# Kernel optimization log

Hardware: AMD Instinct MI355X
Metric: run time of the kernel (lower is better)

## Reference

```python
import jax, jax.numpy as jnp
import numpy as np

N_NODES = 100000


def gcn_conv(h, src, dst, W, b, n_nodes):
    """PyG GCNConv: out = D^{-1/2} (A + I) D^{-1/2} (h W) + b, with added self-loops."""
    h = h @ W  # transform first (in_dim >= out_dim), [N, out]
    # add self loops
    loop = jnp.arange(n_nodes, dtype=src.dtype)
    s = jnp.concatenate([src, loop])
    d = jnp.concatenate([dst, loop])
    # symmetric normalization: deg over destination (col) including self loops
    deg = jax.ops.segment_sum(jnp.ones_like(d, dtype=h.dtype), d, num_segments=n_nodes)
    dinv = jnp.where(deg > 0, jax.lax.rsqrt(deg), 0.0)
    norm = dinv[s] * dinv[d]  # [E+N]
    msg = h[s] * norm[:, None]  # gather + scale, [E+N, out]
    out = jax.ops.segment_sum(msg, d, num_segments=n_nodes)  # scatter-add
    return out + b


def setup_inputs() -> dict:
    key = jax.random.key(0)
    ks = jax.random.split(key, 8)
    n, f, h, o = N_NODES, 128, 32, 16
    x = jax.random.normal(ks[0], (n, f), dtype=jnp.float32)
    edge_index = jax.random.randint(ks[1], (2, 3200000), 0, n, dtype=jnp.int64)
    # Glorot-style init for conv weights, standard linear for head
    W1 = jax.random.normal(ks[2], (f, h), dtype=jnp.float32) * (1.0 / np.sqrt(f))
    b1 = jnp.zeros((h,), dtype=jnp.float32)
    W2 = jax.random.normal(ks[3], (h, o), dtype=jnp.float32) * (1.0 / np.sqrt(h))
    b2 = jnp.zeros((o,), dtype=jnp.float32)
    Wo = jax.random.normal(ks[4], (o, 1), dtype=jnp.float32) * (1.0 / np.sqrt(o))
    bo = jnp.zeros((1,), dtype=jnp.float32)
    return {"x": x, "edge_index": edge_index, "W1": W1, "b1": b1,
            "W2": W2, "b2": b2, "Wo": Wo, "bo": bo}


def reference(x, edge_index, W1, b1, W2, b2, Wo, bo):
    src, dst = edge_index[0], edge_index[1]
    h = jax.nn.relu(gcn_conv(x, src, dst, W1, b1, N_NODES))
    # dropout(p=0.2) is identity in eval mode (training=False)
    h = jax.nn.relu(gcn_conv(h, src, dst, W2, b2, N_NODES))
    return h @ Wo + bo  # [N, 1]
```

## Files before the change

### kernel.cpp

```cpp
#include <hip/hip_runtime.h>

#define F_IN 128
#define H1 32
#define H2 16
#define NPB 128
#define NBKT 782
#define CAP 4608
#define EPT 16
#define BZB 1024
#define EPB (EPT * BZB)

typedef __attribute__((ext_vector_type(8))) short bf16x8;
typedef __attribute__((ext_vector_type(4))) float f32x4;

__device__ inline short bf_hi(float f) { return (short)(__float_as_uint(f) >> 16); }
__device__ inline float bf_to_f(short h) {
    return __uint_as_float(((unsigned)(unsigned short)h) << 16);
}
__device__ inline unsigned short bf_rn(float f) {
    unsigned u = __float_as_uint(f);
    return (unsigned short)((u + 0x7FFFu + ((u >> 16) & 1u)) >> 16);
}
__device__ inline float blo(unsigned u) { return __uint_as_float(u << 16); }
__device__ inline float bhi(unsigned u) { return __uint_as_float(u & 0xFFFF0000u); }

__global__ void k_initcur(int* bucketCur, int nbkt) {
    int b = blockIdx.x * blockDim.x + threadIdx.x;
    if (b < nbkt) bucketCur[b] = b * CAP;
}

__global__ __launch_bounds__(1024) void k_bucketize(const int* __restrict__ src,
        const int* __restrict__ dst, int E,
        int* __restrict__ bucketCur, unsigned* __restrict__ packed) {
    __shared__ int lcnt[NBKT + 1];
    __shared__ int lbase[NBKT];
    int t = threadIdx.x;
    for (int b = t; b < NBKT + 1; b += BZB) lcnt[b] = 0;
    __syncthreads();
    int base = blockIdx.x * EPB;
    int eLast = E - 1;
    unsigned val[EPT]; short bk[EPT]; short rk[EPT];
    #pragma unroll
    for (int i = 0; i < EPT; ++i) {
        int e = base + t + i * BZB;
        int ec = e <= eLast ? e : eLast;
        int s = src[ec], d = dst[ec];
        int b = d >> 7;
        bool ok = e <= eLast;
        bk[i] = ok ? (short)b : (short)-1;
        val[i] = ((unsigned)(d & 127) << 17) | (unsigned)s;
        rk[i] = (short)atomicAdd(&lcnt[ok ? b : NBKT], 1);
    }
    __syncthreads();
    for (int b = t; b < NBKT; b += BZB) {
        int c = lcnt[b];
        if (c > 0) lbase[b] = atomicAdd(&bucketCur[b], c);
    }
    __syncthreads();
    #pragma unroll
    for (int i = 0; i < EPT; ++i)
        if (bk[i] >= 0) packed[lbase[bk[i]] + (int)rk[i]] = val[i];
}

__global__ __launch_bounds__(512) void k_sortbkt(const int* __restrict__ bucketCur,
        const unsigned* __restrict__ packed, unsigned* __restrict__ sorted,
        int* __restrict__ nodeBeg, int* __restrict__ cnt, float* __restrict__ dinv,
        int n) {
    __shared__ int hcnt[NPB];
    __shared__ int hoff[NPB];
    __shared__ int hbase[NPB];
    int b = blockIdx.x, t = threadIdx.x;
    if (t < NPB) hcnt[t] = 0;
    __syncthreads();
    int beg = b * CAP, end = bucketCur[b];
    for (int i = beg + t; i < end; i += 512)
        atomicAdd(&hcnt[packed[i] >> 17], 1);
    __syncthreads();
    if (t < NPB) hoff[t] = hcnt[t];
    __syncthreads();
    #pragma unroll
    for (int off = 1; off < NPB; off <<= 1) {
        int x = (t < NPB && t >= off) ? hoff[t - off] : 0;
        __syncthreads();
        if (t < NPB) hoff[t] += x;
        __syncthreads();
    }
    if (t < NPB) {
        int excl = hoff[t] - hcnt[t];
        hbase[t] = excl;
        int v = b * NPB + t;
        if (v < n) {
            nodeBeg[v] = beg + excl;
            cnt[v] = hcnt[t];
            dinv[v] = rsqrtf((float)hcnt[t] + 1.0f);
        }
    }
    __syncthreads();
    if (t < NPB) hoff[t] = hbase[t];
    __syncthreads();
    for (int i = beg + t; i < end; i += 512) {
        unsigned p = packed[i];
        int dl = p >> 17;
        int r = atomicAdd(&hoff[dl], 1);
        sorted[beg + r] = p & 0x1FFFF;
    }
}

__global__ __launch_bounds__(256) void k_gemm1(const float* __restrict__ x,
        const float* __restrict__ W1, const float* __restrict__ dinv,
        unsigned* __restrict__ g1b, int n) {
    int wave = threadIdx.x >> 6;
    int lane = threadIdx.x & 63;
    int r = lane & 15, kg = lane >> 4;
    int base = blockIdx.x * 64 + wave * 16;
    int node = base + r;
    bool vnode = node < n;
    int nodec = vnode ? node : (n - 1);

    bf16x8 bh[2][4], bl[2][4];
    #pragma unroll
    for (int jt = 0; jt < 2; ++jt) {
        #pragma unroll
        for (int t = 0; t < 4; ++t) {
            #pragma unroll
            for (int i = 0; i < 8; ++i) {
                float w = W1[(t * 32 + kg * 8 + i) * H1 + jt * 16 + r];
                short h = bf_hi(w);
                bh[jt][t][i] = h;
                bl[jt][t][i] = bf_hi(w - bf_to_f(h));
            }
        }
    }

    bf16x8 ah[4], al[4];
    const float4* x4 = (const float4*)x;
    #pragma unroll
    for (int t = 0; t < 4; ++t) {
        float4 a0 = x4[(size_t)nodec * 32 + t * 8 + kg * 2];
        float4 a1 = x4[(size_t)nodec * 32 + t * 8 + kg * 2 + 1];
        float f[8] = {a0.x, a0.y, a0.z, a0.w, a1.x, a1.y, a1.z, a1.w};
        #pragma unroll
        for (int i = 0; i < 8; ++i) {
            float v = vnode ? f[i] : 0.f;
            short h = bf_hi(v);
            ah[t][i] = h;
            al[t][i] = bf_hi(v - bf_to_f(h));
        }
    }

    f32x4 acc[2] = {{0.f, 0.f, 0.f, 0.f}, {0.f, 0.f, 0.f, 0.f}};
    #pragma unroll
    for (int t = 0; t < 4; ++t) {
        #pragma unroll
        for (int jt = 0; jt < 2; ++jt) {
            acc[jt] = __builtin_amdgcn_mfma_f32_16x16x32_bf16(ah[t], bh[jt][t], acc[jt], 0, 0, 0);
            acc[jt] = __builtin_amdgcn_mfma_f32_16x16x32_bf16(al[t], bh[jt][t], acc[jt], 0, 0, 0);
            acc[jt] = __builtin_amdgcn_mfma_f32_16x16x32_bf16(ah[t], bl[jt][t], acc[jt], 0, 0, 0);
        }
    }

    #pragma unroll
    for (int i = 0; i < 4; ++i) {
        int orow = base + kg * 4 + i;
        int oc = orow < n ? orow : 0;
        float dv = dinv[oc];
        float f0 = dv * acc[0][i];
        float f1 = dv * acc[1][i];
        float p0 = __shfl_xor(f0, 1);
        float p1 = __shfl_xor(f1, 1);
        if (orow < n && !(r & 1)) {
            g1b[(size_t)orow * 16 + (r >> 1)]     = (unsigned)bf_rn(f0) | ((unsigned)bf_rn(p0) << 16);
            g1b[(size_t)orow * 16 + 8 + (r >> 1)] = (unsigned)bf_rn(f1) | ((unsigned)bf_rn(p1) << 16);
        }
    }
}

__global__ __launch_bounds__(512) void k_agg1(const int* __restrict__ nodeBeg,
        const int* __restrict__ cnt, const unsigned* __restrict__ sorted,
        const unsigned* __restrict__ g1b, const float* __restrict__ dinv,
        const float* __restrict__ b1, float* __restrict__ h1, int n) {
    int t = threadIdx.x;
    int v = (blockIdx.x * 512 + t) >> 6;
    if (v >= n) return;
    int lane = t & 63;
    int jg = lane & 3, es = lane >> 2;
    int beg = nodeBeg[v], deg = cnt[v];
    const uint4* g4 = (const uint4*)g1b;
    float a0 = 0.f, a1 = 0.f, a2 = 0.f, a3 = 0.f;
    float a4 = 0.f, a5 = 0.f, a6 = 0.f, a7 = 0.f;
    int lastI = deg - 1;
    for (int it = 0; it < deg; it += 32) {
        int i0 = it + es;
        int i1 = it + 16 + es;
        float k0 = i0 <= lastI ? 1.f : 0.f;
        float k1 = i1 <= lastI ? 1.f : 0.f;
        unsigned s0 = sorted[beg + (i0 <= lastI ? i0 : lastI)];
        unsigned s1 = sorted[beg + (i1 <= lastI ? i1 : lastI)];
        uint4 w0 = g4[(size_t)s0 * 4 + jg];
        uint4 w1 = g4[(size_t)s1 * 4 + jg];
        a0 = fmaf(blo(w0.x), k0, a0); a1 = fmaf(bhi(w0.x), k0, a1);
        a2 = fmaf(blo(w0.y), k0, a2); a3 = fmaf(bhi(w0.y), k0, a3);
        a4 = fmaf(blo(w0.z), k0, a4); a5 = fmaf(bhi(w0.z), k0, a5);
        a6 = fmaf(blo(w0.w), k0, a6); a7 = fmaf(bhi(w0.w), k0, a7);
        a0 = fmaf(blo(w1.x), k1, a0); a1 = fmaf(bhi(w1.x), k1, a1);
        a2 = fmaf(blo(w1.y), k1, a2); a3 = fmaf(bhi(w1.y), k1, a3);
        a4 = fmaf(blo(w1.z), k1, a4); a5 = fmaf(bhi(w1.z), k1, a5);
        a6 = fmaf(blo(w1.w), k1, a6); a7 = fmaf(bhi(w1.w), k1, a7);
    }
    #pragma unroll
    for (int m = 4; m < 64; m <<= 1) {
        a0 += __shfl_xor(a0, m); a1 += __shfl_xor(a1, m);
        a2 += __shfl_xor(a2, m); a3 += __shfl_xor(a3, m);
        a4 += __shfl_xor(a4, m); a5 += __shfl_xor(a5, m);
        a6 += __shfl_xor(a6, m); a7 += __shfl_xor(a7, m);
    }
    if (es == 0) {
        uint4 sw = g4[(size_t)v * 4 + jg];
        a0 += blo(sw.x); a1 += bhi(sw.x);
        a2 += blo(sw.y); a3 += bhi(sw.y);
        a4 += blo(sw.z); a5 += bhi(sw.z);
        a6 += blo(sw.w); a7 += bhi(sw.w);
        float dv = dinv[v];
        float4 bb0 = ((const float4*)b1)[jg * 2];
        float4 bb1 = ((const float4*)b1)[jg * 2 + 1];
        float4 r0, r1;
        r0.x = dv * a0 + bb0.x; r0.y = dv * a1 + bb0.y;
        r0.z = dv * a2 + bb0.z; r0.w = dv * a3 + bb0.w;
        r1.x = dv * a4 + bb1.x; r1.y = dv * a5 + bb1.y;
        r1.z = dv * a6 + bb1.z; r1.w = dv * a7 + bb1.w;
        r0.x = r0.x > 0.f ? r0.x : 0.f; r0.y = r0.y > 0.f ? r0.y : 0.f;
        r0.z = r0.z > 0.f ? r0.z : 0.f; r0.w = r0.w > 0.f ? r0.w : 0.f;
        r1.x = r1.x > 0.f ? r1.x : 0.f; r1.y = r1.y > 0.f ? r1.y : 0.f;
        r1.z = r1.z > 0.f ? r1.z : 0.f; r1.w = r1.w > 0.f ? r1.w : 0.f;
        ((float4*)h1)[(size_t)v * 8 + jg * 2]     = r0;
        ((float4*)h1)[(size_t)v * 8 + jg * 2 + 1] = r1;
    }
}

__global__ void k_gemm2(const float* __restrict__ h1, const float* __restrict__ W2,
                        const float* __restrict__ dinv, unsigned* __restrict__ g2b, int n) {
    __shared__ float Wl[H1 * H2];
    for (int t = threadIdx.x; t < H1 * H2; t += blockDim.x) Wl[t] = W2[t];
    __syncthreads();
    int idx = blockIdx.x * blockDim.x + threadIdx.x;
    int node = idx >> 4, j = idx & 15;
    float f = 0.f;
    if (node < n) {
        const float* hr = h1 + (size_t)node * H1;
        float s = 0.f;
        #pragma unroll
        for (int k = 0; k < H1; ++k) s += hr[k] * Wl[k * H2 + j];
        f = dinv[node] * s;
    }
    float p = __shfl_down(f, 1);
    if (node < n && !(j & 1))
        g2b[(size_t)node * 8 + (j >> 1)] = (unsigned)bf_rn(f) | ((unsigned)bf_rn(p) << 16);
}

__global__ __launch_bounds__(512) void k_agg2(const int* __restrict__ nodeBeg,
        const int* __restrict__ cnt, const unsigned* __restrict__ sorted,
        const unsigned* __restrict__ g2b, const float* __restrict__ dinv,
        const float* __restrict__ b2, const float* __restrict__ Wo,
        const float* __restrict__ bo, float* __restrict__ out, int n) {
    int t = threadIdx.x;
    int v = (blockIdx.x * 512 + t) >> 6;
    if (v >= n) return;
    int lane = t & 63;
    int jg = lane & 1, es = lane >> 1;
    int beg = nodeBeg[v], deg = cnt[v];
    const uint4* g4 = (const uint4*)g2b;
    float a0 = 0.f, a1 = 0.f, a2 = 0.f, a3 = 0.f;
    float a4 = 0.f, a5 = 0.f, a6 = 0.f, a7 = 0.f;
    int lastI = deg - 1;
    for (int it = 0; it < deg; it += 64) {
        int i0 = it + es;
        int i1 = it + 32 + es;
        float k0 = i0 <= lastI ? 1.f : 0.f;
        float k1 = i1 <= lastI ? 1.f : 0.f;
        unsigned s0 = sorted[beg + (i0 <= lastI ? i0 : lastI)];
        unsigned s1 = sorted[beg + (i1 <= lastI ? i1 : lastI)];
        uint4 w0 = g4[(size_t)s0 * 2 + jg];
        uint4 w1 = g4[(size_t)s1 * 2 + jg];
        a0 = fmaf(blo(w0.x), k0, a0); a1 = fmaf(bhi(w0.x), k0, a1);
        a2 = fmaf(blo(w0.y), k0, a2); a3 = fmaf(bhi(w0.y), k0, a3);
        a4 = fmaf(blo(w0.z), k0, a4); a5 = fmaf(bhi(w0.z), k0, a5);
        a6 = fmaf(blo(w0.w), k0, a6); a7 = fmaf(bhi(w0.w), k0, a7);
        a0 = fmaf(blo(w1.x), k1, a0); a1 = fmaf(bhi(w1.x), k1, a1);
        a2 = fmaf(blo(w1.y), k1, a2); a3 = fmaf(bhi(w1.y), k1, a3);
        a4 = fmaf(blo(w1.z), k1, a4); a5 = fmaf(bhi(w1.z), k1, a5);
        a6 = fmaf(blo(w1.w), k1, a6); a7 = fmaf(bhi(w1.w), k1, a7);
    }
    #pragma unroll
    for (int m = 2; m < 64; m <<= 1) {
        a0 += __shfl_xor(a0, m); a1 += __shfl_xor(a1, m);
        a2 += __shfl_xor(a2, m); a3 += __shfl_xor(a3, m);
        a4 += __shfl_xor(a4, m); a5 += __shfl_xor(a5, m);
        a6 += __shfl_xor(a6, m); a7 += __shfl_xor(a7, m);
    }
    uint4 sw = g4[(size_t)v * 2 + jg];
    a0 += blo(sw.x); a1 += bhi(sw.x);
    a2 += blo(sw.y); a3 += bhi(sw.y);
    a4 += blo(sw.z); a5 += bhi(sw.z);
    a6 += blo(sw.w); a7 += bhi(sw.w);
    float dv = dinv[v];
    float4 bb0 = ((const float4*)b2)[jg * 2];
    float4 bb1 = ((const float4*)b2)[jg * 2 + 1];
    float4 ww0 = ((const float4*)Wo)[jg * 2];
    float4 ww1 = ((const float4*)Wo)[jg * 2 + 1];
    float q0 = dv * a0 + bb0.x, q1 = dv * a1 + bb0.y;
    float q2 = dv * a2 + bb0.z, q3 = dv * a3 + bb0.w;
    float q4 = dv * a4 + bb1.x, q5 = dv * a5 + bb1.y;
    float q6 = dv * a6 + bb1.z, q7 = dv * a7 + bb1.w;
    float r = (q0 > 0.f ? q0 : 0.f) * ww0.x
            + (q1 > 0.f ? q1 : 0.f) * ww0.y
            + (q2 > 0.f ? q2 : 0.f) * ww0.z
            + (q3 > 0.f ? q3 : 0.f) * ww0.w
            + (q4 > 0.f ? q4 : 0.f) * ww1.x
            + (q5 > 0.f ? q5 : 0.f) * ww1.y
            + (q6 > 0.f ? q6 : 0.f) * ww1.z
            + (q7 > 0.f ? q7 : 0.f) * ww1.w;
    r += __shfl_xor(r, 1);
    if (lane == 0) out[v] = r + bo[0];
}

extern "C" void kernel_launch(void* const* d_in, const int* in_sizes, int n_in,
                              void* d_out, int out_size, void* d_ws, size_t ws_size,
                              hipStream_t stream) {
    const float* x  = (const float*)d_in[0];
    const int*   ei = (const int*)d_in[1];
    const float* W1 = (const float*)d_in[2];
    const float* b1 = (const float*)d_in[3];
    const float* W2 = (const float*)d_in[4];
    const float* b2 = (const float*)d_in[5];
    const float* Wo = (const float*)d_in[6];
    const float* bo = (const float*)d_in[7];
    float* out = (float*)d_out;

    const int n = in_sizes[0] / F_IN;
    const int E = in_sizes[1] / 2;
    const int* src = ei;
    const int* dst = ei + E;
    const int nbkt = (n + NPB - 1) / NPB;

    auto align = [](size_t s) { return (s + 255) & ~(size_t)255; };
    char* ws = (char*)d_ws;
    size_t o = 0;
    int*      cnt      = (int*)(ws + o); o += align((size_t)n * 4);
    float*    dinv     = (float*)(ws + o); o += align((size_t)n * 4);
    int*      nodeBeg  = (int*)(ws + o); o += align((size_t)n * 4);
    int*      bucketCur= (int*)(ws + o); o += align((size_t)nbkt * 4);
    unsigned* packed   = (unsigned*)(ws + o); o += align((size_t)nbkt * CAP * 4);
    unsigned* sorted   = (unsigned*)(ws + o); o += align((size_t)nbkt * CAP * 4);
    unsigned* g1b      = (unsigned*)(ws + o); o += align((size_t)n * 16 * 4);
    float*    h1       = (float*)(ws + o); o += align((size_t)n * H1 * 4);
    unsigned* g2b      = g1b;

    const int B = 256;
    const int aggBlocks = (n * 64 + 511) / 512;
    k_initcur  <<<(nbkt + B - 1) / B, B, 0, stream>>>(bucketCur, nbkt);
    k_bucketize<<<(E + EPB - 1) / EPB, BZB, 0, stream>>>(src, dst, E, bucketCur, packed);
    k_sortbkt  <<<nbkt, 512, 0, stream>>>(bucketCur, packed, sorted, nodeBeg, cnt, dinv, n);
    k_gemm1    <<<(n + 63) / 64, 256, 0, stream>>>(x, W1, dinv, g1b, n);
    k_agg1     <<<aggBlocks, 512, 0, stream>>>(nodeBeg, cnt, sorted, g1b, dinv, b1, h1, n);
    k_gemm2    <<<(n * H2 + B - 1) / B, B, 0, stream>>>(h1, W2, dinv, g2b, n);
    k_agg2     <<<aggBlocks, 512, 0, stream>>>(nodeBeg, cnt, sorted, g2b, dinv, b2, Wo, bo, out, n);
}
```

Measured before the change: 176.5 us.

## Keep bucket records in registers during sort; use half-wave per node in agg2

```diff
diff --git a/kernel.cpp b/kernel.cpp
--- a/kernel.cpp
+++ b/kernel.cpp
@@ -9,6 +9,7 @@
 #define EPT 16
 #define BZB 1024
 #define EPB (EPT * BZB)
+#define RPT 9
 
 typedef __attribute__((ext_vector_type(8))) short bf16x8;
 typedef __attribute__((ext_vector_type(4))) float f32x4;
@@ -73,8 +74,17 @@
     if (t < NPB) hcnt[t] = 0;
     __syncthreads();
     int beg = b * CAP, end = bucketCur[b];
-    for (int i = beg + t; i < end; i += 512)
-        atomicAdd(&hcnt[packed[i] >> 17], 1);
+    unsigned recs[RPT]; unsigned short rks[RPT];
+    #pragma unroll
+    for (int k = 0; k < RPT; ++k) {
+        int i = beg + t + k * 512;
+        bool ok = i < end;
+        int ic = ok ? i : beg;
+        unsigned p = packed[ic];
+        recs[k] = ok ? p : 0xFFFFFFFFu;
+        rks[k] = 0;
+        if (ok) rks[k] = (unsigned short)atomicAdd(&hcnt[p >> 17], 1);
+    }
     __syncthreads();
     if (t < NPB) hoff[t] = hcnt[t];
     __syncthreads();
@@ -96,13 +106,12 @@
         }
     }
     __syncthreads();
-    if (t < NPB) hoff[t] = hbase[t];
-    __syncthreads();
-    for (int i = beg + t; i < end; i += 512) {
-        unsigned p = packed[i];
-        int dl = p >> 17;
-        int r = atomicAdd(&hoff[dl], 1);
-        sorted[beg + r] = p & 0x1FFFF;
+    #pragma unroll
+    for (int k = 0; k < RPT; ++k) {
+        if (recs[k] != 0xFFFFFFFFu) {
+            int dl = recs[k] >> 17;
+            sorted[beg + hbase[dl] + (int)rks[k]] = recs[k] & 0x1FFFF;
+        }
     }
 }
 
@@ -263,18 +272,18 @@
         const float* __restrict__ b2, const float* __restrict__ Wo,
         const float* __restrict__ bo, float* __restrict__ out, int n) {
     int t = threadIdx.x;
-    int v = (blockIdx.x * 512 + t) >> 6;
+    int v = (blockIdx.x * 512 + t) >> 5;
     if (v >= n) return;
-    int lane = t & 63;
-    int jg = lane & 1, es = lane >> 1;
+    int l = t & 31;
+    int jg = l & 1, es = l >> 1;
     int beg = nodeBeg[v], deg = cnt[v];
     const uint4* g4 = (const uint4*)g2b;
     float a0 = 0.f, a1 = 0.f, a2 = 0.f, a3 = 0.f;
     float a4 = 0.f, a5 = 0.f, a6 = 0.f, a7 = 0.f;
     int lastI = deg - 1;
-    for (int it = 0; it < deg; it += 64) {
+    for (int it = 0; it < deg; it += 32) {
         int i0 = it + es;
-        int i1 = it + 32 + es;
+        int i1 = it + 16 + es;
         float k0 = i0 <= lastI ? 1.f : 0.f;
         float k1 = i1 <= lastI ? 1.f : 0.f;
         unsigned s0 = sorted[beg + (i0 <= lastI ? i0 : lastI)];
@@ -291,36 +300,38 @@
         a6 = fmaf(blo(w1.w), k1, a6); a7 = fmaf(bhi(w1.w), k1, a7);
     }
     #pragma unroll
-    for (int m = 2; m < 64; m <<= 1) {
+    for (int m = 2; m < 32; m <<= 1) {
         a0 += __shfl_xor(a0, m); a1 += __shfl_xor(a1, m);
         a2 += __shfl_xor(a2, m); a3 += __shfl_xor(a3, m);
         a4 += __shfl_xor(a4, m); a5 += __shfl_xor(a5, m);
         a6 += __shfl_xor(a6, m); a7 += __shfl_xor(a7, m);
     }
-    uint4 sw = g4[(size_t)v * 2 + jg];
-    a0 += blo(sw.x); a1 += bhi(sw.x);
-    a2 += blo(sw.y); a3 += bhi(sw.y);
-    a4 += blo(sw.z); a5 += bhi(sw.z);
-    a6 += blo(sw.w); a7 += bhi(sw.w);
-    float dv = dinv[v];
-    float4 bb0 = ((const float4*)b2)[jg * 2];
-    float4 bb1 = ((const float4*)b2)[jg * 2 + 1];
-    float4 ww0 = ((const float4*)Wo)[jg * 2];
-    float4 ww1 = ((const float4*)Wo)[jg * 2 + 1];
-    float q0 = dv * a0 + bb0.x, q1 = dv * a1 + bb0.y;
-    float q2 = dv * a2 + bb0.z, q3 = dv * a3 + bb0.w;
-    float q4 = dv * a4 + bb1.x, q5 = dv * a5 + bb1.y;
-    float q6 = dv * a6 + bb1.z, q7 = dv * a7 + bb1.w;
-    float r = (q0 > 0.f ? q0 : 0.f) * ww0.x
-            + (q1 > 0.f ? q1 : 0.f) * ww0.y
-            + (q2 > 0.f ? q2 : 0.f) * ww0.z
-            + (q3 > 0.f ? q3 : 0.f) * ww0.w
-            + (q4 > 0.f ? q4 : 0.f) * ww1.x
-            + (q5 > 0.f ? q5 : 0.f) * ww1.y
-            + (q6 > 0.f ? q6 : 0.f) * ww1.z
-            + (q7 > 0.f ? q7 : 0.f) * ww1.w;
-    r += __shfl_xor(r, 1);
-    if (lane == 0) out[v] = r + bo[0];
+    if (es == 0) {
+        uint4 sw = g4[(size_t)v * 2 + jg];
+        a0 += blo(sw.x); a1 += bhi(sw.x);
+        a2 += blo(sw.y); a3 += bhi(sw.y);
+        a4 += blo(sw.z); a5 += bhi(sw.z);
+        a6 += blo(sw.w); a7 += bhi(sw.w);
+        float dv = dinv[v];
+        float4 bb0 = ((const float4*)b2)[jg * 2];
+        float4 bb1 = ((const float4*)b2)[jg * 2 + 1];
+        float4 ww0 = ((const float4*)Wo)[jg * 2];
+        float4 ww1 = ((const float4*)Wo)[jg * 2 + 1];
+        float q0 = dv * a0 + bb0.x, q1 = dv * a1 + bb0.y;
+        float q2 = dv * a2 + bb0.z, q3 = dv * a3 + bb0.w;
+        float q4 = dv * a4 + bb1.x, q5 = dv * a5 + bb1.y;
+        float q6 = dv * a6 + bb1.z, q7 = dv * a7 + bb1.w;
+        float r = (q0 > 0.f ? q0 : 0.f) * ww0.x
+                + (q1 > 0.f ? q1 : 0.f) * ww0.y
+                + (q2 > 0.f ? q2 : 0.f) * ww0.z
+                + (q3 > 0.f ? q3 : 0.f) * ww0.w
+                + (q4 > 0.f ? q4 : 0.f) * ww1.x
+                + (q5 > 0.f ? q5 : 0.f) * ww1.y
+                + (q6 > 0.f ? q6 : 0.f) * ww1.z
+                + (q7 > 0.f ? q7 : 0.f) * ww1.w;
+        r += __shfl_xor(r, 1);
+        if (l == 0) out[v] = r + bo[0];
+    }
 }
 
 extern "C" void kernel_launch(void* const* d_in, const int* in_sizes, int n_in,
@@ -356,12 +367,13 @@
     unsigned* g2b      = g1b;
 
     const int B = 256;
-    const int aggBlocks = (n * 64 + 511) / 512;
+    const int agg1Blocks = (n * 64 + 511) / 512;
+    const int agg2Blocks = (n * 32 + 511) / 512;
     k_initcur  <<<(nbkt + B - 1) / B, B, 0, stream>>>(bucketCur, nbkt);
     k_bucketize<<<(E + EPB - 1) / EPB, BZB, 0, stream>>>(src, dst, E, bucketCur, packed);
     k_sortbkt  <<<nbkt, 512, 0, stream>>>(bucketCur, packed, sorted, nodeBeg, cnt, dinv, n);
     k_gemm1    <<<(n + 63) / 64, 256, 0, stream>>>(x, W1, dinv, g1b, n);
-    k_agg1     <<<aggBlocks, 512, 0, stream>>>(nodeBeg, cnt, sorted, g1b, dinv, b1, h1, n);
+    k_agg1     <<<agg1Blocks, 512, 0, stream>>>(nodeBeg, cnt, sorted, g1b, dinv, b1, h1, n);
     k_gemm2    <<<(n * H2 + B - 1) / B, B, 0, stream>>>(h1, W2, dinv, g2b, n);
-    k_agg2     <<<aggBlocks, 512, 0, stream>>>(nodeBeg, cnt, sorted, g2b, dinv, b2, Wo, bo, out, n);
-}
+    k_agg2     <<<agg2Blocks, 512, 0, stream>>>(nodeBeg, cnt, sorted, g2b, dinv, b2, Wo, bo, out, n);
+}
```

Result: faster. 159.6 us (-9.6%).
